# Kernel optimization log

Hardware: AMD Instinct MI355X
Metric: run time of the kernel (lower is better)

Reference implementation:

```python
import jax, jax.numpy as jnp
import numpy as np
import math


def setup_inputs() -> dict:
    key = jax.random.key(0)
    k1, k2, k3, k4 = jax.random.split(key, 4)
    b, h, T, dk = 1, 8, 4096, 64
    BS = 64
    T_q = 2048
    num_blocks = T // BS
    q = jax.random.normal(k1, (b, h, T_q, dk), dtype=jnp.float32)
    k = jax.random.normal(k2, (b, h, T, dk), dtype=jnp.float32)
    v = jax.random.normal(k3, (b, h, T, dk), dtype=jnp.float32)
    top2_idx = jax.random.randint(k4, (b, h, T_q, 2), 0, num_blocks, dtype=jnp.int32)
    return {"q": q, "k": k, "v": v, "BS": BS, "top2_idx": top2_idx}


def reference(q, k, v, BS, top2_idx):
    b, h, T, dk = k.shape
    num_blocks = T // BS
    T_q = top2_idx.shape[2]
    # [b,h,num_blocks,BS,dk]
    k_blocks = k.reshape(b, h, num_blocks, BS, dk)
    v_blocks = v.reshape(b, h, num_blocks, BS, dk)
    # gather 2 blocks per query: flat idx [b,h,T_q*2] -> select along block axis
    flat_idx = top2_idx.reshape(b, h, T_q * 2)[..., None, None]  # [b,h,2*T_q,1,1]
    k_sel = jnp.take_along_axis(k_blocks, flat_idx, axis=2).reshape(b, h, T_q, 2 * BS, dk)
    v_sel = jnp.take_along_axis(v_blocks, flat_idx, axis=2).reshape(b, h, T_q, 2 * BS, dk)
    # per-query attention over its 2*BS gathered keys
    score = jnp.einsum("bhqd,bhqkd->bhqk", q, k_sel) / math.sqrt(dk)
    score = jax.nn.softmax(score, axis=-1)
    out = jnp.einsum("bhqk,bhqkd->bhqd", score, v_sel)
    return out
```

## Files before the change

### kernel.cpp

```cpp
#include <hip/hip_runtime.h>


#define NH      8
#define TQ      2048
#define TKV     4096
#define DK      64
#define BSZ     64
#define NB      (TKV / BSZ)
#define NQ_TOT  (NH * TQ)
#define NENT    (NQ_TOT * 2)
#define NBUCKET (NH * NB)
#define SSPLIT  2
#define CAP     256

#define WS_NEEDED    ((size_t)NENT * 68 * 4)

typedef __attribute__((ext_vector_type(8))) short bf16x8;
typedef __attribute__((ext_vector_type(4))) float f32x4;

__device__ __forceinline__ short f2bf(float x) {
    union { float f; unsigned u; } c; c.f = x;
    unsigned r = c.u + 0x7fffu + ((c.u >> 16) & 1u);
    return (short)(r >> 16);
}

__device__ __forceinline__ bf16x8 pack_bf16x8(float4 a, float4 b) {
    bf16x8 r;
    r[0] = f2bf(a.x); r[1] = f2bf(a.y); r[2] = f2bf(a.z); r[3] = f2bf(a.w);
    r[4] = f2bf(b.x); r[5] = f2bf(b.y); r[6] = f2bf(b.z); r[7] = f2bf(b.w);
    return r;
}

#define KSTR 72
#define VSTR 78

__global__ __launch_bounds__(256, 2) void bucket_kernel(
    const float* __restrict__ q,
    const float* __restrict__ k,
    const float* __restrict__ v,
    const int*   __restrict__ top2,
    float*       __restrict__ partials)
{
    __shared__ __align__(16) short K_lds[BSZ * KSTR];
    __shared__ __align__(16) short V_lds[BSZ * VSTR];
    __shared__ __align__(16) short P_lds[4][16 * 72];
    __shared__ int lds_list[CAP];
    __shared__ int wave_tot[4];

    const int bucket  = blockIdx.x & (NBUCKET - 1);
    const int subtile = blockIdx.x >> 9;
    const int wave = threadIdx.x >> 6;
    const int lane = threadIdx.x & 63;
    const int W    = subtile * 4 + wave;

    const int h    = bucket >> 6;
    const int blk  = bucket & (NB - 1);

    const int* th = top2 + h * (TQ * 2);
    int cnt = 0;
#pragma unroll
    for (int rep = 0; rep < (TQ * 2) / 256; ++rep) {
        if ((th[rep * 256 + threadIdx.x] & (NB - 1)) == blk) ++cnt;
    }
    int pre = cnt;
#pragma unroll
    for (int off = 1; off < 64; off <<= 1) {
        const int nb = __shfl_up(pre, off);
        if (lane >= off) pre += nb;
    }
    if (lane == 63) wave_tot[wave] = pre;
    __syncthreads();
    int wbase = 0;
#pragma unroll
    for (int wv = 0; wv < 4; ++wv) if (wv < wave) wbase += wave_tot[wv];
    int nq = wave_tot[0] + wave_tot[1] + wave_tot[2] + wave_tot[3];
    nq = (nq > CAP) ? CAP : nq;
    {
        int p = wbase + pre - cnt;
#pragma unroll
        for (int rep = 0; rep < (TQ * 2) / 256; ++rep) {
            const int i = rep * 256 + threadIdx.x;
            if ((th[i] & (NB - 1)) == blk) {
                if (p < CAP) lds_list[p] = h * (TQ * 2) + i;
                ++p;
            }
        }
    }
    __syncthreads();

    const int ntiles = (nq + 15) >> 4;
    if (ntiles <= subtile * 4) return;

    const int n16  = lane & 15;
    const int quad = lane >> 4;

    const float* kb = k + ((size_t)h * TKV + (size_t)blk * BSZ) * DK;
    const float* vb = v + ((size_t)h * TKV + (size_t)blk * BSZ) * DK;

    {
        const int row = threadIdx.x >> 2;
        const int seg = threadIdx.x & 3;
        const float* kp = kb + row * DK + seg * 16;
        const float* vp = vb + row * DK + seg * 16;
        short* kd = &K_lds[row * KSTR + seg * 16];
        short* vd = &V_lds[row * VSTR + seg * 16];
#pragma unroll
        for (int c = 0; c < 4; ++c) {
            const float4 a = *(const float4*)(kp + c * 4);
            kd[c * 4 + 0] = f2bf(a.x); kd[c * 4 + 1] = f2bf(a.y);
            kd[c * 4 + 2] = f2bf(a.z); kd[c * 4 + 3] = f2bf(a.w);
            const float4 b = *(const float4*)(vp + c * 4);
            vd[c * 4 + 0] = f2bf(b.x); vd[c * 4 + 1] = f2bf(b.y);
            vd[c * 4 + 2] = f2bf(b.z); vd[c * 4 + 3] = f2bf(b.w);
        }
    }
    __syncthreads();
    if (W >= ntiles) return;

    bf16x8 kf[4][2];
#pragma unroll
    for (int kt = 0; kt < 4; ++kt)
#pragma unroll
        for (int ks = 0; ks < 2; ++ks)
            kf[kt][ks] = *(const bf16x8*)&K_lds[(kt * 16 + n16) * KSTR + ks * 32 + quad * 8];

    bf16x8 vf[4][2];
#pragma unroll
    for (int dt = 0; dt < 4; ++dt)
#pragma unroll
        for (int ks = 0; ks < 2; ++ks) {
            bf16x8 t;
#pragma unroll
            for (int jj = 0; jj < 8; ++jj)
                t[jj] = V_lds[(ks * 32 + quad * 8 + jj) * VSTR + dt * 16 + n16];
            vf[dt][ks] = t;
        }

    short* pl = &P_lds[wave][0];

    for (int t = W; t < ntiles; t += 4 * SSPLIT) {
        const int tbase = t * 16;

        const int em_idx = (tbase + n16 < nq) ? (tbase + n16) : 0;
        const int qi = lds_list[em_idx] >> 1;
        bf16x8 qf[2];
#pragma unroll
        for (int ks = 0; ks < 2; ++ks) {
            const float* p = q + (size_t)qi * DK + ks * 32 + quad * 8;
            float4 lo = *(const float4*)p, hi = *(const float4*)(p + 4);
            lo.x *= 0.125f; lo.y *= 0.125f; lo.z *= 0.125f; lo.w *= 0.125f;
            hi.x *= 0.125f; hi.y *= 0.125f; hi.z *= 0.125f; hi.w *= 0.125f;
            qf[ks] = pack_bf16x8(lo, hi);
        }

        f32x4 acc[4];
#pragma unroll
        for (int kt = 0; kt < 4; ++kt) {
            f32x4 a = {0.f, 0.f, 0.f, 0.f};
            a = __builtin_amdgcn_mfma_f32_16x16x32_bf16(qf[0], kf[kt][0], a, 0, 0, 0);
            a = __builtin_amdgcn_mfma_f32_16x16x32_bf16(qf[1], kf[kt][1], a, 0, 0, 0);
            acc[kt] = a;
        }

        float m4[4], l4[4], P[4][4];
#pragma unroll
        for (int r = 0; r < 4; ++r) {
            float mx = fmaxf(fmaxf(acc[0][r], acc[1][r]), fmaxf(acc[2][r], acc[3][r]));
            mx = fmaxf(mx, __shfl_xor(mx, 1));
            mx = fmaxf(mx, __shfl_xor(mx, 2));
            mx = fmaxf(mx, __shfl_xor(mx, 4));
            mx = fmaxf(mx, __shfl_xor(mx, 8));
            float s = 0.f;
#pragma unroll
            for (int kt = 0; kt < 4; ++kt) { P[kt][r] = __expf(acc[kt][r] - mx); s += P[kt][r]; }
            s += __shfl_xor(s, 1);
            s += __shfl_xor(s, 2);
            s += __shfl_xor(s, 4);
            s += __shfl_xor(s, 8);
            m4[r] = mx; l4[r] = s;
        }

#pragma unroll
        for (int r = 0; r < 4; ++r)
#pragma unroll
            for (int kt = 0; kt < 4; ++kt)
                pl[(quad * 4 + r) * 72 + kt * 16 + n16] = f2bf(P[kt][r]);

        bf16x8 pf[2];
#pragma unroll
        for (int ks = 0; ks < 2; ++ks)
            pf[ks] = *(const bf16x8*)&pl[n16 * 72 + ks * 32 + quad * 8];

        f32x4 oacc[4];
#pragma unroll
        for (int dt = 0; dt < 4; ++dt) {
            f32x4 a = {0.f, 0.f, 0.f, 0.f};
            a = __builtin_amdgcn_mfma_f32_16x16x32_bf16(pf[0], vf[dt][0], a, 0, 0, 0);
            a = __builtin_amdgcn_mfma_f32_16x16x32_bf16(pf[1], vf[dt][1], a, 0, 0, 0);
            oacc[dt] = a;
        }

#pragma unroll
        for (int r = 0; r < 4; ++r) {
            const int row = tbase + quad * 4 + r;
            if (row < nq) {
                const int e = lds_list[row];
                float* pp = partials + (size_t)e * 68;
#pragma unroll
                for (int dt = 0; dt < 4; ++dt)
                    pp[dt * 16 + n16] = oacc[dt][r];
                if (n16 == 0) pp[64] = m4[r];
                if (n16 == 1) pp[65] = l4[r];
            }
        }
    }
}

__global__ __launch_bounds__(256) void combine_kernel(
    const float* __restrict__ partials, float* __restrict__ out)
{
    const int t  = blockIdx.x * 256 + threadIdx.x;
    const int qi = t >> 4;
    const int dc = t & 15;
    const float* p0 = partials + (size_t)(qi * 2) * 68;
    const float* p1 = p0 + 68;
    const float m0 = p0[64], l0 = p0[65];
    const float m1 = p1[64], l1 = p1[65];
    const float m  = fmaxf(m0, m1);
    const float a0 = __expf(m0 - m), a1 = __expf(m1 - m);
    const float inv = 1.0f / (a0 * l0 + a1 * l1);
    const float4 o0 = *(const float4*)(p0 + dc * 4);
    const float4 o1 = *(const float4*)(p1 + dc * 4);
    float4 o;
    o.x = (o0.x * a0 + o1.x * a1) * inv;
    o.y = (o0.y * a0 + o1.y * a1) * inv;
    o.z = (o0.z * a0 + o1.z * a1) * inv;
    o.w = (o0.w * a0 + o1.w * a1) * inv;
    *(float4*)(out + (size_t)qi * DK + dc * 4) = o;
}

__global__ __launch_bounds__(256) void blockattn_fallback(
    const float* __restrict__ q, const float* __restrict__ k,
    const float* __restrict__ v, const int* __restrict__ top2,
    float* __restrict__ out)
{
    const int wave = threadIdx.x >> 6;
    const int lane = threadIdx.x & 63;
    const int qidx = (blockIdx.x << 2) + wave;
    const int bh   = qidx >> 11;
    const int g    = lane >> 4;
    const int dc   = lane & 15;

    const int2 idx = *(const int2*)(top2 + (size_t)qidx * 2);
    const size_t bh_off = (size_t)bh * (TKV * DK);
    const int off = g * DK + dc * 4;

    const float* kb0 = k + bh_off + (size_t)idx.x * (BSZ * DK) + off;
    const float* kb1 = k + bh_off + (size_t)idx.y * (BSZ * DK) + off;
    const float* vb0 = v + bh_off + (size_t)idx.x * (BSZ * DK) + off;
    const float* vb1 = v + bh_off + (size_t)idx.y * (BSZ * DK) + off;
    const float4 qf = *(const float4*)(q + (size_t)qidx * DK + dc * 4);

    float sc[32];
#pragma unroll
    for (int i = 0; i < 16; ++i) {
        const float4 a = *(const float4*)(kb0 + i * 256);
        float p = a.x*qf.x + a.y*qf.y + a.z*qf.z + a.w*qf.w;
        p += __shfl_xor(p,1); p += __shfl_xor(p,2); p += __shfl_xor(p,4); p += __shfl_xor(p,8);
        sc[i] = p * 0.125f;
    }
#pragma unroll
    for (int i = 0; i < 16; ++i) {
        const float4 a = *(const float4*)(kb1 + i * 256);
        float p = a.x*qf.x + a.y*qf.y + a.z*qf.z + a.w*qf.w;
        p += __shfl_xor(p,1); p += __shfl_xor(p,2); p += __shfl_xor(p,4); p += __shfl_xor(p,8);
        sc[16+i] = p * 0.125f;
    }
    float m = sc[0];
#pragma unroll
    for (int i = 1; i < 32; ++i) m = fmaxf(m, sc[i]);
    m = fmaxf(m, __shfl_xor(m,16)); m = fmaxf(m, __shfl_xor(m,32));
    float sum = 0.f;
#pragma unroll
    for (int i = 0; i < 32; ++i) { sc[i] = __expf(sc[i]-m); sum += sc[i]; }
    sum += __shfl_xor(sum,16); sum += __shfl_xor(sum,32);
    const float inv = 1.0f / sum;

    float4 acc = make_float4(0.f,0.f,0.f,0.f);
#pragma unroll
    for (int i = 0; i < 16; ++i) {
        const float4 a = *(const float4*)(vb0 + i * 256);
        acc.x += a.x*sc[i]; acc.y += a.y*sc[i]; acc.z += a.z*sc[i]; acc.w += a.w*sc[i];
    }
#pragma unroll
    for (int i = 0; i < 16; ++i) {
        const float4 a = *(const float4*)(vb1 + i * 256);
        acc.x += a.x*sc[16+i]; acc.y += a.y*sc[16+i]; acc.z += a.z*sc[16+i]; acc.w += a.w*sc[16+i];
    }
    acc.x += __shfl_xor(acc.x,16); acc.y += __shfl_xor(acc.y,16);
    acc.z += __shfl_xor(acc.z,16); acc.w += __shfl_xor(acc.w,16);
    acc.x += __shfl_xor(acc.x,32); acc.y += __shfl_xor(acc.y,32);
    acc.z += __shfl_xor(acc.z,32); acc.w += __shfl_xor(acc.w,32);

    if (g == 0) {
        float4 o;
        o.x = acc.x*inv; o.y = acc.y*inv; o.z = acc.z*inv; o.w = acc.w*inv;
        *(float4*)(out + (size_t)qidx * DK + dc * 4) = o;
    }
}

extern "C" void kernel_launch(void* const* d_in, const int* in_sizes, int n_in,
                              void* d_out, int out_size, void* d_ws, size_t ws_size,
                              hipStream_t stream) {
    const float* q    = (const float*)d_in[0];
    const float* k    = (const float*)d_in[1];
    const float* v    = (const float*)d_in[2];
    const int*   top2 = (const int*)d_in[4];
    float*       out  = (float*)d_out;

    if (ws_size < WS_NEEDED) {
        dim3 grid(NQ_TOT / 4), block(256);
        hipLaunchKernelGGL(blockattn_fallback, grid, block, 0, stream, q, k, v, top2, out);
        return;
    }

    float* parts = (float*)d_ws;

    hipLaunchKernelGGL(bucket_kernel,  dim3(NBUCKET * SSPLIT), dim3(256), 0, stream,
                       q, k, v, top2, parts);
    hipLaunchKernelGGL(combine_kernel, dim3(NQ_TOT * 16 / 256), dim3(256), 0, stream,
                       parts, out);
}
```

Baseline: 83.41 us.

## Fuse bucket and combine kernels via cooperative launch with grid sync

Merges the bucket attention kernel and the combine kernel into one cooperative kernel that separates the two phases with a grid-wide barrier. This drops the second launch and its inter-kernel gap. It also removes the 2-way subtile split, so the grid shrinks to one block per bucket and each block walks all of its query tiles alone. That cuts parallelism, leaving long buckets with more serial work, and adds grid-sync overhead. A plain two-kernel launch is kept as a fallback if the cooperative launch fails.

After: 166.3 us. +99.4%, slower.

```diff
diff --git a/kernel.cpp b/kernel.cpp
--- a/kernel.cpp
+++ b/kernel.cpp
@@ -1,5 +1,8 @@
 #include <hip/hip_runtime.h>
-
+#include <hip/hip_cooperative_groups.h>
+
+
+namespace cg = cooperative_groups;
 
 #define NH      8
 #define TQ      2048
@@ -10,7 +13,6 @@
 #define NQ_TOT  (NH * TQ)
 #define NENT    (NQ_TOT * 2)
 #define NBUCKET (NH * NB)
-#define SSPLIT  2
 #define CAP     256
 
 #define WS_NEEDED    ((size_t)NENT * 68 * 4)
@@ -34,24 +36,19 @@
 #define KSTR 72
 #define VSTR 78
 
-__global__ __launch_bounds__(256, 2) void bucket_kernel(
+__device__ __forceinline__ void bucket_phase(
     const float* __restrict__ q,
     const float* __restrict__ k,
     const float* __restrict__ v,
     const int*   __restrict__ top2,
-    float*       __restrict__ partials)
-{
-    __shared__ __align__(16) short K_lds[BSZ * KSTR];
-    __shared__ __align__(16) short V_lds[BSZ * VSTR];
-    __shared__ __align__(16) short P_lds[4][16 * 72];
-    __shared__ int lds_list[CAP];
-    __shared__ int wave_tot[4];
-
-    const int bucket  = blockIdx.x & (NBUCKET - 1);
-    const int subtile = blockIdx.x >> 9;
+    float*       __restrict__ partials,
+    int bucket,
+    short* K_lds, short* V_lds, short* P_lds_all,
+    int* lds_list, int* wave_tot)
+{
     const int wave = threadIdx.x >> 6;
     const int lane = threadIdx.x & 63;
-    const int W    = subtile * 4 + wave;
+    const int W    = wave;
 
     const int h    = bucket >> 6;
     const int blk  = bucket & (NB - 1);
@@ -89,7 +86,7 @@
     __syncthreads();
 
     const int ntiles = (nq + 15) >> 4;
-    if (ntiles <= subtile * 4) return;
+    if (ntiles == 0) return;
 
     const int n16  = lane & 15;
     const int quad = lane >> 4;
@@ -136,9 +133,9 @@
             vf[dt][ks] = t;
         }
 
-    short* pl = &P_lds[wave][0];
-
-    for (int t = W; t < ntiles; t += 4 * SSPLIT) {
+    short* pl = P_lds_all + wave * (16 * 72);
+
+    for (int t = W; t < ntiles; t += 4) {
         const int tbase = t * 16;
 
         const int em_idx = (tbase + n16 < nq) ? (tbase + n16) : 0;
@@ -216,10 +213,9 @@
     }
 }
 
-__global__ __launch_bounds__(256) void combine_kernel(
-    const float* __restrict__ partials, float* __restrict__ out)
-{
-    const int t  = blockIdx.x * 256 + threadIdx.x;
+__device__ __forceinline__ void combine_item(
+    int t, const float* __restrict__ partials, float* __restrict__ out)
+{
     const int qi = t >> 4;
     const int dc = t & 15;
     const float* p0 = partials + (size_t)(qi * 2) * 68;
@@ -239,6 +235,53 @@
     *(float4*)(out + (size_t)qi * DK + dc * 4) = o;
 }
 
+__global__ __launch_bounds__(256, 2) void fused_kernel(
+    const float* __restrict__ q,
+    const float* __restrict__ k,
+    const float* __restrict__ v,
+    const int*   __restrict__ top2,
+    float*       __restrict__ partials,
+    float*       __restrict__ out)
+{
+    __shared__ __align__(16) short K_lds[BSZ * KSTR];
+    __shared__ __align__(16) short V_lds[BSZ * VSTR];
+    __shared__ __align__(16) short P_lds[4 * 16 * 72];
+    __shared__ int lds_list[CAP];
+    __shared__ int wave_tot[4];
+
+    bucket_phase(q, k, v, top2, partials, blockIdx.x,
+                 K_lds, V_lds, P_lds, lds_list, wave_tot);
+
+    cg::this_grid().sync();
+
+    const int nth = gridDim.x * 256;
+    for (int t = blockIdx.x * 256 + threadIdx.x; t < NQ_TOT * 16; t += nth)
+        combine_item(t, partials, out);
+}
+
+__global__ __launch_bounds__(256, 2) void bucket_kernel(
+    const float* __restrict__ q,
+    const float* __restrict__ k,
+    const float* __restrict__ v,
+    const int*   __restrict__ top2,
+    float*       __restrict__ partials)
+{
+    __shared__ __align__(16) short K_lds[BSZ * KSTR];
+    __shared__ __align__(16) short V_lds[BSZ * VSTR];
+    __shared__ __align__(16) short P_lds[4 * 16 * 72];
+    __shared__ int lds_list[CAP];
+    __shared__ int wave_tot[4];
+
+    bucket_phase(q, k, v, top2, partials, blockIdx.x,
+                 K_lds, V_lds, P_lds, lds_list, wave_tot);
+}
+
+__global__ __launch_bounds__(256) void combine_kernel(
+    const float* __restrict__ partials, float* __restrict__ out)
+{
+    combine_item(blockIdx.x * 256 + threadIdx.x, partials, out);
+}
+
 __global__ __launch_bounds__(256) void blockattn_fallback(
     const float* __restrict__ q, const float* __restrict__ k,
     const float* __restrict__ v, const int* __restrict__ top2,
@@ -326,8 +369,15 @@
 
     float* parts = (float*)d_ws;
 
-    hipLaunchKernelGGL(bucket_kernel,  dim3(NBUCKET * SSPLIT), dim3(256), 0, stream,
-                       q, k, v, top2, parts);
-    hipLaunchKernelGGL(combine_kernel, dim3(NQ_TOT * 16 / 256), dim3(256), 0, stream,
-                       parts, out);
-}
+    void* args[] = { (void*)&q, (void*)&k, (void*)&v, (void*)&top2,
+                     (void*)&parts, (void*)&out };
+    hipError_t err = hipLaunchCooperativeKernel(
+        (const void*)fused_kernel, dim3(NBUCKET), dim3(256), args, 0, stream);
+
+    if (err != hipSuccess) {
+        hipLaunchKernelGGL(bucket_kernel,  dim3(NBUCKET), dim3(256), 0, stream,
+                           q, k, v, top2, parts);
+        hipLaunchKernelGGL(combine_kernel, dim3(NQ_TOT * 16 / 256), dim3(256), 0, stream,
+                           parts, out);
+    }
+}
```
